# Kernel optimization log

Hardware: AMD Instinct MI355X
Metric: run time of the kernel (lower is better)

Reference implementation:

```python
import jax, jax.numpy as jnp
import numpy as np

# SLAYER neuron / simulation constants (from params)
THETA = 10.0      # spike threshold
TAU_SR = 10.0     # PSP (synaptic response) time constant
TS = 1.0          # simulation time step
TAU_RHO = 1.0     # surrogate-gradient width
SCALE_RHO = 1.0   # surrogate-gradient scale
ALPHA = float(np.exp(-TS / TAU_SR))  # leaky-filter decay per step

B, C_IN, T = 32, 156, 2048
HID, OUT = 512, 20


@jax.custom_vjp
def spike(u):
    # Hard threshold with SLAYER-style exponential surrogate gradient.
    return (u >= THETA).astype(u.dtype)

def _spike_fwd(u):
    return spike(u), u

def _spike_bwd(u, g):
    sg = (SCALE_RHO / TAU_RHO) * jnp.exp(-jnp.abs(u - THETA) / TAU_RHO)
    return (g * sg,)

spike.defvjp(_spike_fwd, _spike_bwd)


def psp(x):
    # Leaky exponential temporal filter along the LAST axis (SLAYER psp):
    # y[t] = ALPHA * y[t-1] + x[t]
    xt = jnp.moveaxis(x, -1, 0)  # [T, ...]
    def step(c, xi):
        c = ALPHA * c + xi
        return c, c
    _, y = jax.lax.scan(step, jnp.zeros_like(xt[0]), xt)
    return jnp.moveaxis(y, 0, -1)


def dense(x, W):
    # SLAYER dense layer: per-timestep fully-connected over channel dim.
    # x: [N, C, H, W, T], W: [O, C] -> [N, O, H, W, T]
    return jnp.einsum('oc,nchwt->nohwt', W, x)


def _make_perm():
    rng = np.random.default_rng(0)
    random_list = rng.permutation(np.arange(1, 40))
    perm = []
    for i in random_list:
        perm.append(2 * int(i) - 2)
        perm.append(2 * int(i) - 1)
    for i in random_list:
        perm.append(2 * int(i) - 2 + 78)
        perm.append(2 * int(i) - 1 + 78)
    return jnp.asarray(perm, dtype=jnp.int32)


def setup_inputs() -> dict:
    key = jax.random.key(0)
    k0, k1, k2, k3, k4 = jax.random.split(key, 5)
    spike_input = jax.random.randint(k0, (B, C_IN, 1, 1, T), 0, 2).astype(jnp.float32)
    W1 = jax.random.normal(k1, (HID, C_IN), dtype=jnp.float32) * (C_IN ** -0.5)
    W2 = jax.random.normal(k2, (OUT, HID), dtype=jnp.float32) * (HID ** -0.5)
    Wl1 = jax.random.normal(k3, (HID, T), dtype=jnp.float32) * (T ** -0.5)
    Wl2 = jax.random.normal(k4, (OUT, HID), dtype=jnp.float32) * (HID ** -0.5)
    perm = _make_perm()
    return {"spike_input": spike_input, "W1": W1, "W2": W2,
            "Wl1": Wl1, "Wl2": Wl2, "perm": perm}


def reference(spike_input, W1, W2, Wl1, Wl2, perm):
    # Branch 1: channel-dense over taxels, PSP + spike, twice.
    s1 = spike(psp(dense(spike_input, W1)))          # [B, HID, 1, 1, T]
    spike_output = spike(psp(dense(s1, W2)))         # [B, OUT, 1, 1, T]

    # Branch 2: transpose channel<->time, permute taxel axis, dense over time dim.
    x_t = jnp.swapaxes(spike_input, 1, 4)            # [B, T, 1, 1, C_IN]
    x_tp = x_t[..., perm]                            # gather on taxel axis
    l1 = spike(psp(dense(x_tp, Wl1)))                # [B, HID, 1, 1, C_IN]
    location_output = spike(psp(dense(l1, Wl2)))     # [B, OUT, 1, 1, C_IN]

    return jnp.concatenate([spike_output, location_output], axis=4)
```

## Files before the change

kernel.cpp:

```cpp
#include <hip/hip_runtime.h>

#define ALPHA  0.90483741803595952f
#define ALPHA8 0.44932896411722156f
#define THETA  10.0f
#define BF1    ((unsigned short)0x3F80)
#define ISCALE 0.015625f

typedef short   bf16x8 __attribute__((ext_vector_type(8)));
typedef float   f32x4  __attribute__((ext_vector_type(4)));
typedef float   f32x4v __attribute__((ext_vector_type(4)));
typedef unsigned short ushort4v __attribute__((ext_vector_type(4)));
typedef unsigned short ushort8v __attribute__((ext_vector_type(8)));
typedef unsigned char  uchar4v  __attribute__((ext_vector_type(4)));
typedef unsigned char  uchar8v  __attribute__((ext_vector_type(8)));
typedef long long i64;

__device__ __forceinline__ unsigned short f2bf(float f) {
    unsigned int x = __float_as_uint(f);
    unsigned int r = (x + 0x7FFFu + ((x >> 16) & 1u)) >> 16;
    return (unsigned short)r;
}
__device__ __forceinline__ float bf2f(unsigned short h) {
    return __uint_as_float(((unsigned int)h) << 16);
}
__device__ __forceinline__ void split2(float w, unsigned short& h0,
                                       unsigned short& h1) {
    h0 = f2bf(w);          float r0 = w - bf2f(h0);
    h1 = f2bf(r0);
}
__device__ __forceinline__ unsigned char f2fp8(float f) {
    int pk = __builtin_amdgcn_cvt_pk_fp8_f32(f, 0.f, 0, false);
    return (unsigned char)(pk & 0xFF);
}
__device__ __forceinline__ float fp82f(unsigned char b) {
    return __builtin_amdgcn_cvt_f32_fp8((int)b, 0);
}

__global__ __launch_bounds__(256) void prep_scan_pack(
    const float* __restrict__ In, unsigned char* __restrict__ Infp8,
    unsigned short* __restrict__ Pbf,
    const float* __restrict__ W1,  const float* __restrict__ W2,
    const float* __restrict__ Wl1, const float* __restrict__ Wl2,
    unsigned short* __restrict__ W1p,  unsigned char* __restrict__ W2p8,
    unsigned char* __restrict__ Wl1p8, unsigned short* __restrict__ Wl2p)
{
    const int blk = blockIdx.x;
    if (blk >= 4992) {
        const int bidx = blk - 4992;
        if (bidx >= 512 && bidx < 544) {
            int m = bidx - 512;
            for (int k = threadIdx.x; k < 512; k += 256) {
                float w = (m < 20) ? W2[(long long)m * 512 + k] : 0.f;
                unsigned char h0 = f2fp8(w);
                unsigned char h1 = f2fp8(w - fp82f(h0));
                W2p8[(long long)m * 512 + k] = h0;
                W2p8[16384 + (long long)m * 512 + k] = h1;
            }
        } else if (bidx >= 544 && bidx < 1056) {
            int m = bidx - 544;
            for (int k = threadIdx.x; k < 2048; k += 256) {
                float w = Wl1[(long long)m * 2048 + k] * 64.0f;
                unsigned char h0 = f2fp8(w);
                unsigned char h1 = f2fp8(w - fp82f(h0));
                Wl1p8[(long long)m * 2048 + k] = h0;
                Wl1p8[1048576 + (long long)m * 2048 + k] = h1;
            }
        } else {
            const float* W; unsigned short* P; int M, K, Kp, Mp, m;
            if (bidx < 512) { W = W1;  P = W1p;  M = 512; K = 156; Kp = 160; Mp = 512; m = bidx; }
            else            { W = Wl2; P = Wl2p; M = 20;  K = 512; Kp = 512; Mp = 32;  m = bidx - 1056; }
            for (int k = threadIdx.x; k < Kp; k += 256) {
                float v = (m < M && k < K) ? W[(long long)m * K + k] : 0.f;
                unsigned short h0, h1;
                split2(v, h0, h1);
                P[(long long)m * Kp + k] = h0;
                P[(long long)Mp * Kp + (long long)m * Kp + k] = h1;
            }
        }
        return;
    }

    const int row = blk;
    const int tid = threadIdx.x;
    const float* x = In + (long long)row * 2048 + tid * 8;
    const unsigned char ONE8 = f2fp8(1.0f);

    float v[8];
    *(f32x4v*)&v[0] = *(const f32x4v*)x;
    *(f32x4v*)&v[4] = *(const f32x4v*)(x + 4);

    uchar8v raw;
    #pragma unroll
    for (int k = 0; k < 8; ++k) raw[k] = (v[k] >= 0.5f) ? ONE8 : (unsigned char)0;
    *(uchar8v*)(Infp8 + (long long)row * 2048 + tid * 8) = raw;

    float y = 0.f;
    #pragma unroll
    for (int k = 0; k < 8; ++k) { y = ALPHA * y + v[k]; v[k] = y; }

    __shared__ float sc[256];
    float val = y;
    sc[tid] = val;
    float m = ALPHA8;
    for (int d = 1; d < 256; d <<= 1) {
        __syncthreads();
        float p = (tid >= d) ? sc[tid - d] : 0.f;
        __syncthreads();
        val += m * p;
        sc[tid] = val;
        m *= m;
    }
    __syncthreads();
    float carry = (tid > 0) ? sc[tid - 1] : 0.f;

    ushort8v pv;
    float ak = ALPHA;
    #pragma unroll
    for (int k = 0; k < 8; ++k) {
        float yk = v[k] + ak * carry;
        ak *= ALPHA;
        pv[k] = f2bf(yk);
    }
    *(ushort8v*)(Pbf + (long long)row * 2048 + tid * 8) = pv;
}

__global__ __launch_bounds__(256) void transposeP(
    const unsigned short* __restrict__ Pbf, unsigned short* __restrict__ PT)
{
    __shared__ unsigned short Tile[64][72];
    const int t0 = blockIdx.x * 64;
    const int c0 = blockIdx.y * 64;
    const int b  = blockIdx.z;
    const int tid = threadIdx.x;

    #pragma unroll
    for (int s = 0; s < 2; ++s) {
        int id = tid + s * 256;
        int cc = id >> 3;
        int t8 = (id & 7) * 8;
        ushort8v v = {0,0,0,0,0,0,0,0};
        if (c0 + cc < 156)
            v = *(const ushort8v*)(Pbf + (long long)(b * 156 + c0 + cc) * 2048 + t0 + t8);
        *(ushort8v*)&Tile[cc][t8] = v;
    }
    __syncthreads();

    #pragma unroll
    for (int s = 0; s < 2; ++s) {
        int id = tid + s * 256;
        int t  = id >> 3;
        int c8 = (id & 7) * 8;
        if (c0 + c8 + 7 < 160) {
            unsigned short r[8];
            #pragma unroll
            for (int j = 0; j < 8; ++j) r[j] = Tile[c8 + j][t];
            *(ushort8v*)(PT + (long long)b * 327680 + (long long)(t0 + t) * 160 + c0 + c8)
                = *(ushort8v*)r;
        }
    }
}

__global__ __launch_bounds__(256) void mega_gemm1(
    const unsigned short* __restrict__ W1p,
    const unsigned short* __restrict__ PT,
    unsigned short* __restrict__ S1bits,
    const unsigned char* __restrict__ Wl1p8,
    const unsigned char* __restrict__ Infp8,
    unsigned short* __restrict__ Zp)
{
    __shared__ alignas(16) unsigned char SMEM[30720];
    const int bx  = blockIdx.x;
    const int tid = threadIdx.x;
    const int lane = tid & 63, w = tid >> 6;
    const int wy = w >> 1, wx = w & 1;
    const int l15 = lane & 15, kq = lane >> 4;

    if (bx < 2048) {
        auto As = (unsigned short (*)[128][40])SMEM;
        auto Bs = (unsigned short (*)[40])(SMEM + 20480);

        const int z  = bx >> 6;
        const int m0 = ((bx >> 4) & 3) * 128;
        const int n0 = (bx & 15) * 128;
        const unsigned short* Tb = PT + (long long)z * 327680;

        int aPl[4], aM[4], aK8[4];
        #pragma unroll
        for (int s = 0; s < 4; ++s) {
            int id = tid + s * 256;
            aPl[s] = id >> 9; int rem = id & 511;
            aM[s] = rem >> 2; aK8[s] = (rem & 3) * 8;
        }
        int bT[2], bC8[2];
        #pragma unroll
        for (int s = 0; s < 2; ++s) {
            int id = tid + s * 256;
            bT[s] = id >> 2; bC8[s] = (id & 3) * 8;
        }

        f32x4 acc[4][4] = {};
        ushort8v aReg[4], bReg[2];

        #pragma unroll
        for (int s = 0; s < 4; ++s)
            aReg[s] = *(const ushort8v*)(W1p + (long long)aPl[s] * 81920 +
                                         (long long)(m0 + aM[s]) * 160 + aK8[s]);
        #pragma unroll
        for (int s = 0; s < 2; ++s)
            bReg[s] = *(const ushort8v*)(Tb + (long long)(n0 + bT[s]) * 160 + bC8[s]);
        #pragma unroll
        for (int s = 0; s < 4; ++s) *(ushort8v*)&As[aPl[s]][aM[s]][aK8[s]] = aReg[s];
        #pragma unroll
        for (int s = 0; s < 2; ++s) *(ushort8v*)&Bs[bT[s]][bC8[s]] = bReg[s];
        __syncthreads();

        #pragma unroll
        for (int it = 0; it < 5; ++it) {
            const int kn = (it + 1) * 32;
            if (it < 4) {
                #pragma unroll
                for (int s = 0; s < 4; ++s)
                    aReg[s] = *(const ushort8v*)(W1p + (long long)aPl[s] * 81920 +
                                                 (long long)(m0 + aM[s]) * 160 + kn + aK8[s]);
                #pragma unroll
                for (int s = 0; s < 2; ++s)
                    bReg[s] = *(const ushort8v*)(Tb + (long long)(n0 + bT[s]) * 160 + kn + bC8[s]);
            }

            bf16x8 bfr[4];
            #pragma unroll
            for (int nt = 0; nt < 4; ++nt)
                bfr[nt] = *(const bf16x8*)&Bs[wx * 64 + nt * 16 + l15][kq * 8];
            #pragma unroll
            for (int s = 0; s < 2; ++s) {
                #pragma unroll
                for (int mt = 0; mt < 4; ++mt) {
                    bf16x8 afr = *(const bf16x8*)&As[s][wy * 64 + mt * 16 + l15][kq * 8];
                    #pragma unroll
                    for (int nt = 0; nt < 4; ++nt)
                        acc[mt][nt] = __builtin_amdgcn_mfma_f32_16x16x32_bf16(
                            afr, bfr[nt], acc[mt][nt], 0, 0, 0);
                }
            }
            __syncthreads();
            if (it < 4) {
                #pragma unroll
                for (int s = 0; s < 4; ++s) *(ushort8v*)&As[aPl[s]][aM[s]][aK8[s]] = aReg[s];
                #pragma unroll
                for (int s = 0; s < 2; ++s) *(ushort8v*)&Bs[bT[s]][bC8[s]] = bReg[s];
                __syncthreads();
            }
        }

        unsigned short* Db = S1bits + (long long)z * 512 * 128;
        #pragma unroll
        for (int mt = 0; mt < 4; ++mt) {
            #pragma unroll
            for (int i = 0; i < 4; ++i) {
                int m = m0 + wy * 64 + mt * 16 + kq * 4 + i;
                #pragma unroll
                for (int nt = 0; nt < 4; ++nt) {
                    unsigned long long mask = __ballot(acc[mt][nt][i] >= THETA);
                    if (l15 == 0) {
                        int nchunk = (n0 + wx * 64 + nt * 16) >> 4;
                        Db[(long long)m * 128 + nchunk] =
                            (unsigned short)((mask >> (kq * 16)) & 0xFFFFu);
                    }
                }
            }
        }
    } else {
        auto As8 = (unsigned char (*)[64][72])SMEM;
        auto Bs8 = (unsigned char (*)[72])(SMEM + 9216);

        const int id0 = bx - 2048;
        const int nIdx = id0 % 40;
        if (nIdx >= 39) return;
        const int rest = id0 / 40;
        const int n0  = nIdx * 128;
        const int m0  = (rest & 7) * 64;
        const int ksl = rest >> 3;
        const int ks0 = ksl * 512;

        int aPl[4], aM[4], aK8[4];
        #pragma unroll
        for (int s = 0; s < 4; ++s) {
            int id = tid + s * 256;
            aPl[s] = id >> 9; int rem = id & 511;
            aM[s] = rem >> 3; aK8[s] = (rem & 7) * 8;
        }
        int bN[4], bK8[4];
        #pragma unroll
        for (int s = 0; s < 4; ++s) {
            int id = tid + s * 256;
            bN[s] = id >> 3; bK8[s] = (id & 7) * 8;
        }

        f32x4 acc[2][4] = {};
        uchar8v aReg[4], bReg[4];

        #pragma unroll
        for (int s = 0; s < 4; ++s)
            aReg[s] = *(const uchar8v*)(Wl1p8 + (long long)aPl[s] * 1048576 +
                                        (long long)(m0 + aM[s]) * 2048 + ks0 + aK8[s]);
        #pragma unroll
        for (int s = 0; s < 4; ++s)
            bReg[s] = *(const uchar8v*)(Infp8 + (long long)(n0 + bN[s]) * 2048 + ks0 + bK8[s]);
        #pragma unroll
        for (int s = 0; s < 4; ++s) *(uchar8v*)&As8[aPl[s]][aM[s]][aK8[s]] = aReg[s];
        #pragma unroll
        for (int s = 0; s < 4; ++s) *(uchar8v*)&Bs8[bN[s]][bK8[s]] = bReg[s];
        __syncthreads();

        for (int it = 0; it < 8; ++it) {
            const int kn = ks0 + (it + 1) * 64;
            if (it < 7) {
                #pragma unroll
                for (int s = 0; s < 4; ++s)
                    aReg[s] = *(const uchar8v*)(Wl1p8 + (long long)aPl[s] * 1048576 +
                                                (long long)(m0 + aM[s]) * 2048 + kn + aK8[s]);
                #pragma unroll
                for (int s = 0; s < 4; ++s)
                    bReg[s] = *(const uchar8v*)(Infp8 + (long long)(n0 + bN[s]) * 2048 + kn + bK8[s]);
            }

            #pragma unroll
            for (int ks = 0; ks < 2; ++ks) {
                i64 bfr[4];
                #pragma unroll
                for (int nt = 0; nt < 4; ++nt)
                    bfr[nt] = *(const i64*)&Bs8[wx * 64 + nt * 16 + l15][ks * 32 + kq * 8];
                #pragma unroll
                for (int s = 0; s < 2; ++s) {
                    #pragma unroll
                    for (int mt = 0; mt < 2; ++mt) {
                        i64 afr = *(const i64*)&As8[s][wy * 32 + mt * 16 + l15][ks * 32 + kq * 8];
                        #pragma unroll
                        for (int nt = 0; nt < 4; ++nt)
                            acc[mt][nt] = __builtin_amdgcn_mfma_f32_16x16x32_fp8_fp8(
                                afr, bfr[nt], acc[mt][nt], 0, 0, 0);
                    }
                }
            }
            __syncthreads();
            if (it < 7) {
                #pragma unroll
                for (int s = 0; s < 4; ++s) *(uchar8v*)&As8[aPl[s]][aM[s]][aK8[s]] = aReg[s];
                #pragma unroll
                for (int s = 0; s < 4; ++s) *(uchar8v*)&Bs8[bN[s]][bK8[s]] = bReg[s];
                __syncthreads();
            }
        }

        unsigned short* Tu = (unsigned short*)SMEM;
        #pragma unroll
        for (int mt = 0; mt < 2; ++mt) {
            #pragma unroll
            for (int i = 0; i < 4; ++i) {
                int mL = wy * 32 + mt * 16 + kq * 4 + i;
                #pragma unroll
                for (int nt = 0; nt < 4; ++nt) {
                    int nL = wx * 64 + nt * 16 + l15;
                    Tu[mL * 129 + nL] = f2bf(acc[mt][nt][i] * ISCALE);
                }
            }
        }
        __syncthreads();

        unsigned short* Zs = Zp + (long long)ksl * 2555904;
        #pragma unroll
        for (int s2 = 0; s2 < 32; ++s2) {
            int id = tid + s2 * 256;
            int cL = id >> 6;
            int mL = id & 63;
            int n = n0 + cL;
            int bb = n / 156, cc = n - bb * 156;
            Zs[(long long)cc * 16384 + bb * 512 + m0 + mL] = Tu[mL * 129 + cL];
        }
    }
}

__global__ __launch_bounds__(256) void mega_stage2(
    const unsigned char* __restrict__ W2p8,
    const unsigned short* __restrict__ S1bits,
    float* __restrict__ C2p,
    const unsigned short* __restrict__ Zp,
    const int* __restrict__ perm,
    unsigned short* __restrict__ L1T)
{
    __shared__ alignas(16) unsigned char SMEM[20608];
    const int bx  = blockIdx.x;
    const int tid = threadIdx.x;

    if (bx < 1024) {
        auto As = (unsigned char (*)[32][72])SMEM;
        auto Bs = (unsigned char (*)[72])(SMEM + 4608);

        const int lane = tid & 63, w = tid >> 6;
        const int l15 = lane & 15, kq = lane >> 4;
        const int n0  = (bx & 15) * 128;
        const int ksl = (bx >> 4) & 1;
        const int b   = bx >> 5;
        const int ks0 = ksl * 256;

        const unsigned short* Bb = S1bits + (long long)b * 512 * 128;
        const unsigned char ONE8 = f2fp8(1.0f);

        int aPl[2], aM[2], aK8[2];
        #pragma unroll
        for (int s = 0; s < 2; ++s) {
            int id = tid + s * 256;
            aPl[s] = id >> 8; int rem = id & 255;
            aM[s] = rem >> 3; aK8[s] = (rem & 7) * 8;
        }
        const int kb = (tid >> 4) * 4;
        const int nb = (tid & 15) * 8;
        const int nchunk = (n0 + nb) >> 4;
        const int nshift = nb & 15;

        f32x4 acc[2][2] = {};
        uchar8v aReg[2];
        unsigned short bBits[4];

        auto loadA = [&](int k0) {
            #pragma unroll
            for (int s = 0; s < 2; ++s)
                aReg[s] = *(const uchar8v*)(W2p8 + (long long)aPl[s] * 16384 +
                                            (long long)aM[s] * 512 + k0 + aK8[s]);
        };
        auto loadB = [&](int k0) {
            #pragma unroll
            for (int kk2 = 0; kk2 < 4; ++kk2)
                bBits[kk2] = Bb[(long long)(k0 + kb + kk2) * 128 + nchunk];
        };
        auto stage = [&]() {
            #pragma unroll
            for (int s = 0; s < 2; ++s) *(uchar8v*)&As[aPl[s]][aM[s]][aK8[s]] = aReg[s];
            unsigned char bv[4][8];
            #pragma unroll
            for (int kk2 = 0; kk2 < 4; ++kk2) {
                unsigned int bits = ((unsigned int)bBits[kk2] >> nshift) & 0xFFu;
                #pragma unroll
                for (int j = 0; j < 8; ++j)
                    bv[kk2][j] = ((bits >> j) & 1u) ? ONE8 : (unsigned char)0;
            }
            #pragma unroll
            for (int j = 0; j < 8; ++j) {
                uchar4v v4 = { bv[0][j], bv[1][j], bv[2][j], bv[3][j] };
                *(uchar4v*)&Bs[nb + j][kb] = v4;
            }
        };

        loadA(ks0); loadB(ks0);
        stage();
        __syncthreads();

        #pragma unroll
        for (int it = 0; it < 4; ++it) {
            const int kn = ks0 + (it + 1) * 64;
            if (it < 3) { loadA(kn); loadB(kn); }

            #pragma unroll
            for (int ks = 0; ks < 2; ++ks) {
                i64 bfr[2];
                #pragma unroll
                for (int nt = 0; nt < 2; ++nt)
                    bfr[nt] = *(const i64*)&Bs[w * 32 + nt * 16 + l15][ks * 32 + kq * 8];
                #pragma unroll
                for (int s = 0; s < 2; ++s) {
                    #pragma unroll
                    for (int mt = 0; mt < 2; ++mt) {
                        i64 afr = *(const i64*)&As[s][mt * 16 + l15][ks * 32 + kq * 8];
                        #pragma unroll
                        for (int nt = 0; nt < 2; ++nt)
                            acc[mt][nt] = __builtin_amdgcn_mfma_f32_16x16x32_fp8_fp8(
                                afr, bfr[nt], acc[mt][nt], 0, 0, 0);
                    }
                }
            }
            __syncthreads();
            if (it < 3) {
                stage();
                __syncthreads();
            }
        }

        float* Cb = C2p + (long long)b * 20 * 2048 + (long long)ksl * 1310720LL;
        #pragma unroll
        for (int mt = 0; mt < 2; ++mt) {
            #pragma unroll
            for (int i = 0; i < 4; ++i) {
                int m = mt * 16 + kq * 4 + i;
                if (m >= 20) continue;
                #pragma unroll
                for (int nt = 0; nt < 2; ++nt) {
                    int n = n0 + w * 32 + nt * 16 + l15;
                    Cb[(long long)m * 2048 + n] = acc[mt][nt][i];
                }
            }
        }
    } else {
        auto Xs = (float (*)[32])SMEM;
        int* p  = (int*)(SMEM + 19968);

        const int r0 = (bx - 1024) * 32;
        for (int i = tid; i < 156; i += 256) p[i] = perm[i];

        const int row = tid & 31;
        const int cq  = tid >> 5;
        #pragma unroll
        for (int it = 0; it < 20; ++it) {
            int c = it * 8 + cq;
            if (c < 156) {
                long long base = (long long)c * 16384 + r0 + row;
                float s = bf2f(Zp[base]) + bf2f(Zp[base + 2555904]) +
                          bf2f(Zp[base + 2 * 2555904]) + bf2f(Zp[base + 3 * 2555904]);
                Xs[c][row] = s;
            }
        }
        __syncthreads();

        if (tid < 32) {
            float y = 0.f;
            for (int c = 0; c < 156; ++c) {
                y = ALPHA * y + Xs[p[c]][tid];
                L1T[(long long)c * 16384 + r0 + tid] = (y >= THETA) ? BF1 : 0;
            }
        }
    }
}

__global__ __launch_bounds__(256) void mega_stage3(
    const float* __restrict__ C2p, float* __restrict__ out,
    const unsigned short* __restrict__ Wl2p,
    const unsigned short* __restrict__ L1T,
    float* __restrict__ Cl2)
{
    __shared__ alignas(16) unsigned char SMEM[27648];
    const int bx  = blockIdx.x;
    const int tid = threadIdx.x;

    if (bx < 640) {
        float* sc = (float*)SMEM;
        const int row = bx;
        const float* x = C2p + (long long)row * 2048 + tid * 8;

        float v[8];
        #pragma unroll
        for (int k = 0; k < 8; ++k) v[k] = x[k] + x[k + 1310720LL];

        float y = 0.f;
        #pragma unroll
        for (int k = 0; k < 8; ++k) { y = ALPHA * y + v[k]; v[k] = y; }

        float val = y;
        sc[tid] = val;
        float m = ALPHA8;
        for (int d = 1; d < 256; d <<= 1) {
            __syncthreads();
            float p = (tid >= d) ? sc[tid - d] : 0.f;
            __syncthreads();
            val += m * p;
            sc[tid] = val;
            m *= m;
        }
        __syncthreads();
        float carry = (tid > 0) ? sc[tid - 1] : 0.f;

        float* o = out + (long long)row * 2204 + tid * 8;
        float ak = ALPHA;
        #pragma unroll
        for (int k = 0; k < 8; ++k) {
            float yk = v[k] + ak * carry;
            ak *= ALPHA;
            o[k] = (yk >= THETA) ? 1.0f : 0.0f;
        }
    } else {
        auto As = (unsigned short (*)[32][72])SMEM;
        auto Bs = (unsigned short (*)[72])(SMEM + 9216);

        const int id2 = bx - 640;
        const int n0 = (id2 & 1) * 128;
        const int b  = id2 >> 1;
        const int lane = tid & 63, w = tid >> 6;
        const int l15 = lane & 15, kq = lane >> 4;

        f32x4 acc[2][2] = {};

        for (int k0 = 0; k0 < 512; k0 += 64) {
            #pragma unroll
            for (int s = 0; s < 2; ++s) {
                int id = tid + s * 256;
                int pl = id >> 8, rem = id & 255;
                int m = rem >> 3, k8 = (rem & 7) * 8;
                ushort8v v = *(const ushort8v*)(Wl2p + (long long)pl * 16384 +
                                                (long long)m * 512 + k0 + k8);
                *(ushort8v*)&As[pl][m][k8] = v;
            }
            #pragma unroll
            for (int s = 0; s < 4; ++s) {
                int id = tid + s * 256;
                int n = id >> 3, k8 = (id & 7) * 8;
                ushort8v v = {0,0,0,0,0,0,0,0};
                if (n0 + n < 156)
                    v = *(const ushort8v*)(L1T + (long long)(n0 + n) * 16384 +
                                           b * 512 + k0 + k8);
                *(ushort8v*)&Bs[n][k8] = v;
            }
            __syncthreads();

            #pragma unroll
            for (int ks = 0; ks < 2; ++ks) {
                bf16x8 bfr[2];
                #pragma unroll
                for (int nt = 0; nt < 2; ++nt)
                    bfr[nt] = *(const bf16x8*)&Bs[w * 32 + nt * 16 + l15][ks * 32 + kq * 8];
                #pragma unroll
                for (int s = 0; s < 2; ++s) {
                    #pragma unroll
                    for (int mt = 0; mt < 2; ++mt) {
                        bf16x8 afr = *(const bf16x8*)&As[s][mt * 16 + l15][ks * 32 + kq * 8];
                        #pragma unroll
                        for (int nt = 0; nt < 2; ++nt)
                            acc[mt][nt] = __builtin_amdgcn_mfma_f32_16x16x32_bf16(
                                afr, bfr[nt], acc[mt][nt], 0, 0, 0);
                    }
                }
            }
            __syncthreads();
        }

        float* Cb = Cl2 + (long long)b * 20 * 156;
        #pragma unroll
        for (int mt = 0; mt < 2; ++mt) {
            #pragma unroll
            for (int i = 0; i < 4; ++i) {
                int m = mt * 16 + kq * 4 + i;
                if (m >= 20) continue;
                #pragma unroll
                for (int nt = 0; nt < 2; ++nt) {
                    int n = n0 + w * 32 + nt * 16 + l15;
                    if (n < 156) Cb[(long long)m * 156 + n] = acc[mt][nt][i];
                }
            }
        }
    }
}

__global__ __launch_bounds__(256) void scan_spike_C_out(
    const float* __restrict__ in, float* __restrict__ out, int rows)
{
    int row = blockIdx.x * blockDim.x + threadIdx.x;
    if (row >= rows) return;
    const float* x = in + (long long)row * 156;
    float* o = out + (long long)row * 2204 + 2048;
    float y = 0.f;
    for (int c = 0; c < 156; ++c) {
        y = ALPHA * y + x[c];
        o[c] = (y >= THETA) ? 1.0f : 0.0f;
    }
}

extern "C" void kernel_launch(void* const* d_in, const int* in_sizes, int n_in,
                              void* d_out, int out_size, void* d_ws, size_t ws_size,
                              hipStream_t stream)
{
    const float* In  = (const float*)d_in[0];
    const float* W1  = (const float*)d_in[1];
    const float* W2  = (const float*)d_in[2];
    const float* Wl1 = (const float*)d_in[3];
    const float* Wl2 = (const float*)d_in[4];
    const int*  perm = (const int*)d_in[5];
    float* out = (float*)d_out;

    float* ws = (float*)d_ws;
    unsigned short* S1bits = (unsigned short*)ws;
    float* C2p = ws + 1048576LL;
    unsigned char*  Infp8 = (unsigned char*)(ws + 3670016LL);
    unsigned short* Pbf  = (unsigned short*)(ws + 6225920LL);
    unsigned short* PT   = (unsigned short*)(ws + 11337728LL);
    unsigned short* W1p  = (unsigned short*)(ws + 16580608LL);
    unsigned char*  W2p8 = (unsigned char*)(ws + 16662528LL);
    unsigned char*  Wl1p8= (unsigned char*)(ws + 16670720LL);
    unsigned short* Wl2p = (unsigned short*)(ws + 17195008LL);
    unsigned short* Zpbf = (unsigned short*)(ws + 17211392LL);
    unsigned short* L1T  = (unsigned short*)(ws + 22323200LL);
    float* Cl2 = ws + 23601152LL;

    dim3 blk(256);

    prep_scan_pack<<<dim3(6080), blk, 0, stream>>>(
        In, Infp8, Pbf, W1, W2, Wl1, Wl2, W1p, W2p8, Wl1p8, Wl2p);
    transposeP<<<dim3(32, 3, 32), blk, 0, stream>>>(Pbf, PT);

    mega_gemm1<<<dim3(3328), blk, 0, stream>>>(W1p, PT, S1bits,
                                               Wl1p8, Infp8, Zpbf);
    mega_stage2<<<dim3(1536), blk, 0, stream>>>(W2p8, S1bits, C2p,
                                                Zpbf, perm, L1T);
    mega_stage3<<<dim3(704), blk, 0, stream>>>(C2p, out, Wl2p, L1T, Cl2);
    scan_spike_C_out<<<dim3(3), blk, 0, stream>>>(Cl2, out, 640);

    (void)in_sizes; (void)n_in; (void)out_size; (void)ws_size;
}
```

Before: 207.2 us.

## Double-buffer LDS in gemm1, shrink its M tile, fuse final scan into stage3

The first GEMM branch now uses 64-row M tiles, which doubles its block count. Both GEMM branches keep two LDS buffers, so the next K tile is staged while the current one is consumed, and each iteration needs one barrier instead of two. Stage3's location branch now covers all 156 columns in a single block per batch and runs the PSP/spike scan from shared memory, which removes the separate scan kernel launch and the Cl2 round trip. The costs are more LDS per block, smaller tiles that reuse the B operand less, and a serial scan run by only 20 threads inside the stage3 blocks.

Result: faster. 191.1 us (-7.8%).

```diff
diff --git a/kernel.cpp b/kernel.cpp
--- a/kernel.cpp
+++ b/kernel.cpp
@@ -160,7 +160,7 @@
     }
 }
 
-__global__ __launch_bounds__(256) void mega_gemm1(
+__global__ __launch_bounds__(256, 4) void mega_gemm1(
     const unsigned short* __restrict__ W1p,
     const unsigned short* __restrict__ PT,
     unsigned short* __restrict__ S1bits,
@@ -168,96 +168,85 @@
     const unsigned char* __restrict__ Infp8,
     unsigned short* __restrict__ Zp)
 {
-    __shared__ alignas(16) unsigned char SMEM[30720];
+    __shared__ alignas(16) unsigned char SMEM[40960];
     const int bx  = blockIdx.x;
     const int tid = threadIdx.x;
     const int lane = tid & 63, w = tid >> 6;
     const int wy = w >> 1, wx = w & 1;
     const int l15 = lane & 15, kq = lane >> 4;
 
-    if (bx < 2048) {
-        auto As = (unsigned short (*)[128][40])SMEM;
-        auto Bs = (unsigned short (*)[40])(SMEM + 20480);
-
-        const int z  = bx >> 6;
-        const int m0 = ((bx >> 4) & 3) * 128;
+    if (bx < 4096) {
+        auto As = (unsigned short (*)[2][64][40])SMEM;
+        auto Bs = (unsigned short (*)[128][40])(SMEM + 20480);
+
+        const int z  = bx >> 7;
+        const int m0 = ((bx >> 4) & 7) * 64;
         const int n0 = (bx & 15) * 128;
         const unsigned short* Tb = PT + (long long)z * 327680;
 
-        int aPl[4], aM[4], aK8[4];
-        #pragma unroll
-        for (int s = 0; s < 4; ++s) {
-            int id = tid + s * 256;
-            aPl[s] = id >> 9; int rem = id & 511;
-            aM[s] = rem >> 2; aK8[s] = (rem & 3) * 8;
-        }
-        int bT[2], bC8[2];
+        int aPl[2], aM[2], aK8[2], bT[2], bC8[2];
         #pragma unroll
         for (int s = 0; s < 2; ++s) {
             int id = tid + s * 256;
-            bT[s] = id >> 2; bC8[s] = (id & 3) * 8;
-        }
-
-        f32x4 acc[4][4] = {};
-        ushort8v aReg[4], bReg[2];
-
-        #pragma unroll
-        for (int s = 0; s < 4; ++s)
-            aReg[s] = *(const ushort8v*)(W1p + (long long)aPl[s] * 81920 +
-                                         (long long)(m0 + aM[s]) * 160 + aK8[s]);
-        #pragma unroll
-        for (int s = 0; s < 2; ++s)
-            bReg[s] = *(const ushort8v*)(Tb + (long long)(n0 + bT[s]) * 160 + bC8[s]);
-        #pragma unroll
-        for (int s = 0; s < 4; ++s) *(ushort8v*)&As[aPl[s]][aM[s]][aK8[s]] = aReg[s];
-        #pragma unroll
-        for (int s = 0; s < 2; ++s) *(ushort8v*)&Bs[bT[s]][bC8[s]] = bReg[s];
+            aPl[s] = id >> 8; int rem = id & 255;
+            aM[s] = rem >> 2; aK8[s] = (rem & 3) * 8;
+            bT[s] = id >> 2;  bC8[s] = (id & 3) * 8;
+        }
+
+        f32x4 acc[2][4] = {};
+        ushort8v aReg[2], bReg[2];
+
+        auto loadAB = [&](int k0) {
+            #pragma unroll
+            for (int s = 0; s < 2; ++s)
+                aReg[s] = *(const ushort8v*)(W1p + (long long)aPl[s] * 81920 +
+                                             (long long)(m0 + aM[s]) * 160 + k0 + aK8[s]);
+            #pragma unroll
+            for (int s = 0; s < 2; ++s)
+                bReg[s] = *(const ushort8v*)(Tb + (long long)(n0 + bT[s]) * 160 + k0 + bC8[s]);
+        };
+        auto stage = [&](int buf) {
+            #pragma unroll
+            for (int s = 0; s < 2; ++s) *(ushort8v*)&As[buf][aPl[s]][aM[s]][aK8[s]] = aReg[s];
+            #pragma unroll
+            for (int s = 0; s < 2; ++s) *(ushort8v*)&Bs[buf][bT[s]][bC8[s]] = bReg[s];
+        };
+
+        loadAB(0);
+        stage(0);
         __syncthreads();
 
         #pragma unroll
         for (int it = 0; it < 5; ++it) {
-            const int kn = (it + 1) * 32;
-            if (it < 4) {
-                #pragma unroll
-                for (int s = 0; s < 4; ++s)
-                    aReg[s] = *(const ushort8v*)(W1p + (long long)aPl[s] * 81920 +
-                                                 (long long)(m0 + aM[s]) * 160 + kn + aK8[s]);
-                #pragma unroll
-                for (int s = 0; s < 2; ++s)
-                    bReg[s] = *(const ushort8v*)(Tb + (long long)(n0 + bT[s]) * 160 + kn + bC8[s]);
-            }
+            const int cur = it & 1;
+            if (it < 4) loadAB((it + 1) * 32);
 
             bf16x8 bfr[4];
             #pragma unroll
             for (int nt = 0; nt < 4; ++nt)
-                bfr[nt] = *(const bf16x8*)&Bs[wx * 64 + nt * 16 + l15][kq * 8];
+                bfr[nt] = *(const bf16x8*)&Bs[cur][wx * 64 + nt * 16 + l15][kq * 8];
             #pragma unroll
             for (int s = 0; s < 2; ++s) {
                 #pragma unroll
-                for (int mt = 0; mt < 4; ++mt) {
-                    bf16x8 afr = *(const bf16x8*)&As[s][wy * 64 + mt * 16 + l15][kq * 8];
+                for (int mt = 0; mt < 2; ++mt) {
+                    bf16x8 afr = *(const bf16x8*)&As[cur][s][wy * 32 + mt * 16 + l15][kq * 8];
                     #pragma unroll
                     for (int nt = 0; nt < 4; ++nt)
                         acc[mt][nt] = __builtin_amdgcn_mfma_f32_16x16x32_bf16(
                             afr, bfr[nt], acc[mt][nt], 0, 0, 0);
                 }
             }
+
+            if (it < 4) stage(cur ^ 1);
             __syncthreads();
-            if (it < 4) {
-                #pragma unroll
-                for (int s = 0; s < 4; ++s) *(ushort8v*)&As[aPl[s]][aM[s]][aK8[s]] = aReg[s];
-                #pragma unroll
-                for (int s = 0; s < 2; ++s) *(ushort8v*)&Bs[bT[s]][bC8[s]] = bReg[s];
-                __syncthreads();
-            }
         }
 
         unsigned short* Db = S1bits + (long long)z * 512 * 128;
         #pragma unroll
-        for (int mt = 0; mt < 4; ++mt) {
+        for (int mt = 0; mt < 2; ++mt) {
             #pragma unroll
             for (int i = 0; i < 4; ++i) {
-                int m = m0 + wy * 64 + mt * 16 + kq * 4 + i;
+                int m = m0 + wy * 32 + mt * 16 + kq * 4 + i;
                 #pragma unroll
                 for (int nt = 0; nt < 4; ++nt) {
                     unsigned long long mask = __ballot(acc[mt][nt][i] >= THETA);
@@ -270,10 +259,10 @@
             }
         }
     } else {
-        auto As8 = (unsigned char (*)[64][72])SMEM;
-        auto Bs8 = (unsigned char (*)[72])(SMEM + 9216);
-
-        const int id0 = bx - 2048;
+        auto As8 = (unsigned char (*)[2][64][72])SMEM;
+        auto Bs8 = (unsigned char (*)[128][72])(SMEM + 18432);
+
+        const int id0 = bx - 4096;
         const int nIdx = id0 % 40;
         if (nIdx >= 39) return;
         const int rest = id0 / 40;
@@ -282,59 +271,53 @@
         const int ksl = rest >> 3;
         const int ks0 = ksl * 512;
 
-        int aPl[4], aM[4], aK8[4];
+        int aPl[4], aM[4], aK8[4], bN[4], bK8[4];
         #pragma unroll
         for (int s = 0; s < 4; ++s) {
             int id = tid + s * 256;
             aPl[s] = id >> 9; int rem = id & 511;
             aM[s] = rem >> 3; aK8[s] = (rem & 7) * 8;
-        }
-        int bN[4], bK8[4];
-        #pragma unroll
-        for (int s = 0; s < 4; ++s) {
-            int id = tid + s * 256;
-            bN[s] = id >> 3; bK8[s] = (id & 7) * 8;
+            bN[s] = id >> 3;  bK8[s] = (id & 7) * 8;
         }
 
         f32x4 acc[2][4] = {};
         uchar8v aReg[4], bReg[4];
 
-        #pragma unroll
-        for (int s = 0; s < 4; ++s)
-            aReg[s] = *(const uchar8v*)(Wl1p8 + (long long)aPl[s] * 1048576 +
-                                        (long long)(m0 + aM[s]) * 2048 + ks0 + aK8[s]);
-        #pragma unroll
-        for (int s = 0; s < 4; ++s)
-            bReg[s] = *(const uchar8v*)(Infp8 + (long long)(n0 + bN[s]) * 2048 + ks0 + bK8[s]);
-        #pragma unroll
-        for (int s = 0; s < 4; ++s) *(uchar8v*)&As8[aPl[s]][aM[s]][aK8[s]] = aReg[s];
-        #pragma unroll
-        for (int s = 0; s < 4; ++s) *(uchar8v*)&Bs8[bN[s]][bK8[s]] = bReg[s];
+        auto loadAB = [&](int k0) {
+            #pragma unroll
+            for (int s = 0; s < 4; ++s)
+                aReg[s] = *(const uchar8v*)(Wl1p8 + (long long)aPl[s] * 1048576 +
+                                            (long long)(m0 + aM[s]) * 2048 + k0 + aK8[s]);
+            #pragma unroll
+            for (int s = 0; s < 4; ++s)
+                bReg[s] = *(const uchar8v*)(Infp8 + (long long)(n0 + bN[s]) * 2048 + k0 + bK8[s]);
+        };
+        auto stage = [&](int buf) {
+            #pragma unroll
+            for (int s = 0; s < 4; ++s) *(uchar8v*)&As8[buf][aPl[s]][aM[s]][aK8[s]] = aReg[s];
+            #pragma unroll
+            for (int s = 0; s < 4; ++s) *(uchar8v*)&Bs8[buf][bN[s]][bK8[s]] = bReg[s];
+        };
+
+        loadAB(ks0);
+        stage(0);
         __syncthreads();
 
         for (int it = 0; it < 8; ++it) {
-            const int kn = ks0 + (it + 1) * 64;
-            if (it < 7) {
-                #pragma unroll
-                for (int s = 0; s < 4; ++s)
-                    aReg[s] = *(const uchar8v*)(Wl1p8 + (long long)aPl[s] * 1048576 +
-                                                (long long)(m0 + aM[s]) * 2048 + kn + aK8[s]);
-                #pragma unroll
-                for (int s = 0; s < 4; ++s)
-                    bReg[s] = *(const uchar8v*)(Infp8 + (long long)(n0 + bN[s]) * 2048 + kn + bK8[s]);
-            }
+            const int cur = it & 1;
+            if (it < 7) loadAB(ks0 + (it + 1) * 64);
 
             #pragma unroll
             for (int ks = 0; ks < 2; ++ks) {
                 i64 bfr[4];
                 #pragma unroll
                 for (int nt = 0; nt < 4; ++nt)
-                    bfr[nt] = *(const i64*)&Bs8[wx * 64 + nt * 16 + l15][ks * 32 + kq * 8];
+                    bfr[nt] = *(const i64*)&Bs8[cur][wx * 64 + nt * 16 + l15][ks * 32 + kq * 8];
                 #pragma unroll
                 for (int s = 0; s < 2; ++s) {
                     #pragma unroll
                     for (int mt = 0; mt < 2; ++mt) {
-                        i64 afr = *(const i64*)&As8[s][wy * 32 + mt * 16 + l15][ks * 32 + kq * 8];
+                        i64 afr = *(const i64*)&As8[cur][s][wy * 32 + mt * 16 + l15][ks * 32 + kq * 8];
                         #pragma unroll
                         for (int nt = 0; nt < 4; ++nt)
                             acc[mt][nt] = __builtin_amdgcn_mfma_f32_16x16x32_fp8_fp8(
@@ -342,14 +325,9 @@
                     }
                 }
             }
+
+            if (it < 7) stage(cur ^ 1);
             __syncthreads();
-            if (it < 7) {
-                #pragma unroll
-                for (int s = 0; s < 4; ++s) *(uchar8v*)&As8[aPl[s]][aM[s]][aK8[s]] = aReg[s];
-                #pragma unroll
-                for (int s = 0; s < 4; ++s) *(uchar8v*)&Bs8[bN[s]][bK8[s]] = bReg[s];
-                __syncthreads();
-            }
         }
 
         unsigned short* Tu = (unsigned short*)SMEM;
@@ -533,10 +511,9 @@
 __global__ __launch_bounds__(256) void mega_stage3(
     const float* __restrict__ C2p, float* __restrict__ out,
     const unsigned short* __restrict__ Wl2p,
-    const unsigned short* __restrict__ L1T,
-    float* __restrict__ Cl2)
+    const unsigned short* __restrict__ L1T)
 {
-    __shared__ alignas(16) unsigned char SMEM[27648];
+    __shared__ alignas(16) unsigned char SMEM[36864];
     const int bx  = blockIdx.x;
     const int tid = threadIdx.x;
 
@@ -579,13 +556,11 @@
         auto As = (unsigned short (*)[32][72])SMEM;
         auto Bs = (unsigned short (*)[72])(SMEM + 9216);
 
-        const int id2 = bx - 640;
-        const int n0 = (id2 & 1) * 128;
-        const int b  = id2 >> 1;
+        const int b  = bx - 640;
         const int lane = tid & 63, w = tid >> 6;
         const int l15 = lane & 15, kq = lane >> 4;
 
-        f32x4 acc[2][2] = {};
+        f32x4 acc[2][3] = {};
 
         for (int k0 = 0; k0 < 512; k0 += 64) {
             #pragma unroll
@@ -598,12 +573,12 @@
                 *(ushort8v*)&As[pl][m][k8] = v;
             }
             #pragma unroll
-            for (int s = 0; s < 4; ++s) {
+            for (int s = 0; s < 6; ++s) {
                 int id = tid + s * 256;
                 int n = id >> 3, k8 = (id & 7) * 8;
                 ushort8v v = {0,0,0,0,0,0,0,0};
-                if (n0 + n < 156)
-                    v = *(const ushort8v*)(L1T + (long long)(n0 + n) * 16384 +
+                if (n < 156)
+                    v = *(const ushort8v*)(L1T + (long long)n * 16384 +
                                            b * 512 + k0 + k8);
                 *(ushort8v*)&Bs[n][k8] = v;
             }
@@ -611,17 +586,17 @@
 
             #pragma unroll
             for (int ks = 0; ks < 2; ++ks) {
-                bf16x8 bfr[2];
-                #pragma unroll
-                for (int nt = 0; nt < 2; ++nt)
-                    bfr[nt] = *(const bf16x8*)&Bs[w * 32 + nt * 16 + l15][ks * 32 + kq * 8];
+                bf16x8 bfr[3];
+                #pragma unroll
+                for (int nt = 0; nt < 3; ++nt)
+                    bfr[nt] = *(const bf16x8*)&Bs[w * 48 + nt * 16 + l15][ks * 32 + kq * 8];
                 #pragma unroll
                 for (int s = 0; s < 2; ++s) {
                     #pragma unroll
                     for (int mt = 0; mt < 2; ++mt) {
                         bf16x8 afr = *(const bf16x8*)&As[s][mt * 16 + l15][ks * 32 + kq * 8];
                         #pragma unroll
-                        for (int nt = 0; nt < 2; ++nt)
+                        for (int nt = 0; nt < 3; ++nt)
                             acc[mt][nt] = __builtin_amdgcn_mfma_f32_16x16x32_bf16(
                                 afr, bfr[nt], acc[mt][nt], 0, 0, 0);
                     }
@@ -630,34 +605,30 @@
             __syncthreads();
         }
 
-        float* Cb = Cl2 + (long long)b * 20 * 156;
+        float* Cs = (float*)SMEM;
         #pragma unroll
         for (int mt = 0; mt < 2; ++mt) {
             #pragma unroll
             for (int i = 0; i < 4; ++i) {
                 int m = mt * 16 + kq * 4 + i;
-                if (m >= 20) continue;
-                #pragma unroll
-                for (int nt = 0; nt < 2; ++nt) {
-                    int n = n0 + w * 32 + nt * 16 + l15;
-                    if (n < 156) Cb[(long long)m * 156 + n] = acc[mt][nt][i];
-                }
-            }
-        }
-    }
-}
-
-__global__ __launch_bounds__(256) void scan_spike_C_out(
-    const float* __restrict__ in, float* __restrict__ out, int rows)
-{
-    int row = blockIdx.x * blockDim.x + threadIdx.x;
-    if (row >= rows) return;
-    const float* x = in + (long long)row * 156;
-    float* o = out + (long long)row * 2204 + 2048;
-    float y = 0.f;
-    for (int c = 0; c < 156; ++c) {
-        y = ALPHA * y + x[c];
-        o[c] = (y >= THETA) ? 1.0f : 0.0f;
+                #pragma unroll
+                for (int nt = 0; nt < 3; ++nt) {
+                    int n = w * 48 + nt * 16 + l15;
+                    Cs[m * 193 + n] = acc[mt][nt][i];
+                }
+            }
+        }
+        __syncthreads();
+
+        if (tid < 20) {
+            const float* cr = Cs + tid * 193;
+            float* o = out + (long long)(b * 20 + tid) * 2204 + 2048;
+            float y = 0.f;
+            for (int c = 0; c < 156; ++c) {
+                y = ALPHA * y + cr[c];
+                o[c] = (y >= THETA) ? 1.0f : 0.0f;
+            }
+        }
     }
 }
 
@@ -685,7 +656,6 @@
     unsigned short* Wl2p = (unsigned short*)(ws + 17195008LL);
     unsigned short* Zpbf = (unsigned short*)(ws + 17211392LL);
     unsigned short* L1T  = (unsigned short*)(ws + 22323200LL);
-    float* Cl2 = ws + 23601152LL;
 
     dim3 blk(256);
 
@@ -693,12 +663,11 @@
         In, Infp8, Pbf, W1, W2, Wl1, Wl2, W1p, W2p8, Wl1p8, Wl2p);
     transposeP<<<dim3(32, 3, 32), blk, 0, stream>>>(Pbf, PT);
 
-    mega_gemm1<<<dim3(3328), blk, 0, stream>>>(W1p, PT, S1bits,
+    mega_gemm1<<<dim3(5376), blk, 0, stream>>>(W1p, PT, S1bits,
                                                Wl1p8, Infp8, Zpbf);
     mega_stage2<<<dim3(1536), blk, 0, stream>>>(W2p8, S1bits, C2p,
                                                 Zpbf, perm, L1T);
-    mega_stage3<<<dim3(704), blk, 0, stream>>>(C2p, out, Wl2p, L1T, Cl2);
-    scan_spike_C_out<<<dim3(3), blk, 0, stream>>>(Cl2, out, 640);
+    mega_stage3<<<dim3(672), blk, 0, stream>>>(C2p, out, Wl2p, L1T);
 
     (void)in_sizes; (void)n_in; (void)out_size; (void)ws_size;
 }
```
